# Performance work log

Measured on AMD Instinct MI355X. Metric: run time of the kernel, lower is better.

## Reference

```python
import jax, jax.numpy as jnp
import numpy as np
from itertools import combinations, product

NQ = 10
DIM = 2 ** NQ
DEPTH = 1
ENC_PAIRS = [(q, q + 1) for q in range(0, NQ - 1, 2)] + [(q, q + 1) for q in range(1, NQ - 1, 2)]  # brick layer: even then odd
PYR = [(i, i + 1) for layer in range(NQ - 1) for i in range(NQ - layer - 1)]  # pyramid RBS wire pairs (45)
OBS_PAIRS = list(combinations(range(NQ), 2))  # 45 pairwise 2-local observables

_P = {'I': np.eye(2, dtype=np.complex128),
      'X': np.array([[0, 1], [1, 0]], dtype=np.complex128),
      'Y': np.array([[0, -1j], [1j, 0]], dtype=np.complex128),
      'Z': np.array([[1, 0], [0, -1]], dtype=np.complex128)}
_WORDS = [''.join(w) for w in product('IXYZ', repeat=2)][1:]  # PennyLane pauli_basis order, identity excluded
P15 = jnp.asarray(np.stack([np.kron(_P[w[0]], _P[w[1]]) for w in _WORDS]).astype(np.complex64))
XXm = jnp.asarray(np.kron(_P['X'], _P['X']).astype(np.complex64))
YYm = jnp.asarray(np.kron(_P['Y'], _P['Y']).astype(np.complex64))
ZZm = jnp.asarray(np.kron(_P['Z'], _P['Z']).astype(np.complex64))
I4 = jnp.eye(4, dtype=jnp.complex64)
_TRIL_I, _TRIL_J = np.tril_indices(4, -1)  # order matches create_Hermitian's count+j indexing


def _u3(t, p, l):
    c = jnp.cos(t / 2).astype(jnp.complex64)
    s = jnp.sin(t / 2).astype(jnp.complex64)
    return jnp.stack([jnp.stack([c, -jnp.exp(1j * l) * s]),
                      jnp.stack([jnp.exp(1j * p) * s, jnp.exp(1j * (p + l)) * c])])


def _ising(phi, P):
    # exp(-i*phi/2 * P) for P in {XX, YY, ZZ} (P^2 = I)
    return jnp.cos(phi / 2) * I4 - 1j * jnp.sin(phi / 2) * P


def _apply1(psi, U, w):
    # psi: (B, 2, ..., 2); single-qubit gate U (2,2) on wire w
    psi = jnp.moveaxis(psi, 1 + w, -1)
    sh = psi.shape
    out = jnp.einsum('ij,brj->bri', U, psi.reshape(sh[0], -1, 2)).reshape(sh)
    return jnp.moveaxis(out, -1, 1 + w)


def _apply2(psi, U, a, b):
    # two-qubit gate on wires (a,b), a is most-significant (PennyLane wire order). U: (4,4) or batched (B,4,4)
    psi = jnp.moveaxis(psi, (1 + a, 1 + b), (-2, -1))
    sh = psi.shape
    flat = psi.reshape(sh[0], -1, 4)
    eq = 'bij,brj->bri' if U.ndim == 3 else 'ij,brj->bri'
    out = jnp.einsum(eq, U, flat).reshape(sh)
    return jnp.moveaxis(out, (-2, -1), (1 + a, 1 + b))


def _build_H(A, B, D):
    # create_Hermitian: lower triangle A+iB, diag[0:3] = D[1:4], diag[3]=0, then h + h^dagger
    n = A.shape[0]
    h = jnp.zeros((n, 4, 4), jnp.complex64)
    h = h.at[:, _TRIL_I, _TRIL_J].set(A.astype(jnp.complex64) + 1j * B.astype(jnp.complex64))
    d = np.arange(3)
    h = h.at[:, d, d].set(D[:, 1:4].astype(jnp.complex64))
    return h + jnp.conj(jnp.swapaxes(h, -1, -2))


def setup_inputs() -> dict:
    key = jax.random.key(0)
    ks = jax.random.split(key, 9)
    f32 = jnp.float32
    return {
        'x': jax.random.normal(ks[0], (256, 512), f32),
        'W1': jax.random.normal(ks[1], (512, 256), f32) * (512 ** -0.5),
        'b1': jnp.zeros((256,), f32),
        'W2': jax.random.normal(ks[2], (256, 135), f32) * (256 ** -0.5),
        'b2': jnp.zeros((135,), f32),
        'qvit_params': 0.01 * jax.random.normal(ks[3], (DEPTH, len(PYR), 12), f32),
        'A': 2.0 * jax.random.normal(ks[4], (len(OBS_PAIRS), 6), f32),
        'B': 2.0 * jax.random.normal(ks[5], (len(OBS_PAIRS), 6), f32),
        'D': 2.0 * jax.random.normal(ks[6], (len(OBS_PAIRS), 4), f32),
    }


def reference(x, W1, b1, W2, b2, qvit_params, A, B, D):
    Bsz = x.shape[0]
    # enc_proj: Linear -> SiLU -> Linear
    enc = jax.nn.silu(x @ W1 + b1) @ W2 + b2  # (B, 135)
    # Brick-layer SpecialUnitary encoding: U = exp(i * sum theta_m P_m) via eigh
    theta = enc.reshape(Bsz, len(ENC_PAIRS), 15).astype(jnp.complex64)
    Hg = jnp.einsum('bgm,mij->bgij', theta, P15)  # Hermitian generators (B, 9, 4, 4)
    ew, V = jnp.linalg.eigh(Hg)
    Ue = jnp.einsum('bgik,bgk,bgjk->bgij', V, jnp.exp(1j * ew.astype(jnp.complex64)), jnp.conj(V))
    # |0...0>
    psi = jnp.zeros((Bsz, DIM), jnp.complex64).at[:, 0].set(1.0).reshape((Bsz,) + (2,) * NQ)
    for g, (a, b) in enumerate(ENC_PAIRS):
        psi = _apply2(psi, Ue[:, g], a, b)
    # QViT pyramid ansatz
    for ly in range(DEPTH):
        for g, (a, b) in enumerate(PYR):
            p = qvit_params[ly, g]
            psi = _apply1(psi, _u3(p[0], p[1], p[2]), a)
            psi = _apply2(psi, _ising(p[3], XXm), a, b)
            psi = _apply2(psi, _ising(p[4], YYm), a, b)
            psi = _apply2(psi, _ising(p[5], ZZm), a, b)
            psi = _apply1(psi, _u3(p[6], p[7], p[8]), a)
            psi = _apply2(psi, _ising(p[9], XXm), a, b)
            psi = _apply2(psi, _ising(p[10], YYm), a, b)
            psi = _apply2(psi, _ising(p[11], ZZm), a, b)
    # Pairwise ANO Hermitian expectations
    Hobs = _build_H(A, B, D)  # (45, 4, 4)
    outs = []
    for w, (a, b) in enumerate(OBS_PAIRS):
        pm = jnp.moveaxis(psi, (1 + a, 1 + b), (1, 2)).reshape(Bsz, 4, -1)
        outs.append(jnp.real(jnp.einsum('bir,ij,bjr->b', jnp.conj(pm), Hobs[w], pm)))
    return jnp.stack(outs, axis=1).astype(jnp.float32)
```

## Files before the change

### kernel.cpp

```cpp
#include <hip/hip_runtime.h>
#include <math.h>

#define NOBS 45
typedef float2 c32;

__device__ __constant__ int PA_s[NOBS] = {
    1,1,1,1,1,1,1,1,1, 0,0,0,0,0,0,0,0, 7,7,7,7,7,7,7, 6,6,6,6,6,6,
    5,5,5,5,5, 3,3,3,3, 2,2,2, 4,4, 9};
__device__ __constant__ int PB_s[NOBS] = {
    0,7,6,5,3,2,4,9,8, 7,6,5,3,2,4,9,8, 6,5,3,2,4,9,8, 5,3,2,4,9,8,
    3,2,4,9,8, 2,4,9,8, 4,9,8, 9,8, 8};
constexpr int TIc[6] = {1, 2, 2, 3, 3, 3};
constexpr int TJc[6] = {0, 0, 1, 0, 1, 2};

__device__ __forceinline__ c32 cfma(c32 a, c32 b, c32 c) {
    c.x = fmaf(a.x, b.x, fmaf(-a.y, b.y, c.x));
    c.y = fmaf(a.x, b.y, fmaf(a.y, b.x, c.y));
    return c;
}
__device__ __forceinline__ c32 cmul(c32 a, c32 b) {
    return make_float2(a.x * b.x - a.y * b.y, a.x * b.y + a.y * b.x);
}

template <int CTRL>
__device__ __forceinline__ float dppf(float x) {
    return __uint_as_float((unsigned)__builtin_amdgcn_update_dpp(
        0, (int)__float_as_uint(x), CTRL, 0xF, 0xF, true));
}
__device__ __forceinline__ float swap32f(float a) {
    auto r = __builtin_amdgcn_permlane32_swap(__float_as_uint(a), __float_as_uint(a), false, false);
    return (__uint_as_float(r[0]) + __uint_as_float(r[1])) - a;
}
#if __has_builtin(__builtin_amdgcn_permlane16_swap)
__device__ __forceinline__ float swap16f(float a) {
    auto r = __builtin_amdgcn_permlane16_swap(__float_as_uint(a), __float_as_uint(a), false, false);
    return (__uint_as_float(r[0]) + __uint_as_float(r[1])) - a;
}
#else
__device__ __forceinline__ float swap16f(float a) { return __shfl_xor(a, 16, 64); }
#endif
__device__ __forceinline__ float swz4f(float a) {
    return __uint_as_float(__builtin_amdgcn_ds_swizzle(__float_as_uint(a), 0x101F));
}
template <int M>
__device__ __forceinline__ float exf(float x) {
    float r = x;
    if constexpr ((M & 3) == 1) r = dppf<0xB1>(r);
    else if constexpr ((M & 3) == 2) r = dppf<0x4E>(r);
    else if constexpr ((M & 3) == 3) r = dppf<0x1B>(r);
    if constexpr (M & 4)  r = swz4f(r);
    if constexpr (M & 8)  r = dppf<0x128>(r);
    if constexpr (M & 16) r = swap16f(r);
    if constexpr (M & 32) r = swap32f(r);
    return r;
}
template <int M>
__device__ __forceinline__ c32 exch(c32 a) { return make_float2(exf<M>(a.x), exf<M>(a.y)); }
__device__ __forceinline__ c32 swap32c(c32 a) { return make_float2(swap32f(a.x), swap32f(a.y)); }

__device__ __forceinline__ float wave_reduce63(float x) {
    x += dppf<0x111>(x);
    x += dppf<0x112>(x);
    x += dppf<0x114>(x);
    x += dppf<0x118>(x);
    x += dppf<0x142>(x);
    x += dppf<0x143>(x);
    return x;
}

__device__ __forceinline__ int insert2(int t, int pl, int ph) {
    int low  = t & ((1 << pl) - 1);
    int rest = t >> pl;
    int nm   = ph - 1 - pl;
    int mid  = rest & ((1 << nm) - 1);
    int high = rest >> nm;
    return low | (mid << (pl + 1)) | (high << (ph + 1));
}

template <int W>
__device__ __forceinline__ c32 pE(int r, int c) {
    if constexpr (W == 0) return make_float2((r == c) ? 1.f : 0.f, 0.f);
    else if constexpr (W == 1) return make_float2((r != c) ? 1.f : 0.f, 0.f);
    else if constexpr (W == 2) return make_float2(0.f, (r == c) ? 0.f : ((r == 0) ? -1.f : 1.f));
    else return make_float2((r == c) ? ((r == 0) ? 1.f : -1.f) : 0.f, 0.f);
}
template <int W0, int W1>
__device__ __forceinline__ void paccum(c32& H, float th, int i1, int i2, int j1, int j2) {
    c32 a = pE<W0>(i1, j1), b = pE<W1>(i2, j2);
    c32 p = cmul(a, b);
    H.x = fmaf(th, p.x, H.x);
    H.y = fmaf(th, p.y, H.y);
}

struct F16 { c32 u[16]; };
struct FLoc { c32 a[4]; c32 b[4]; };
struct F4 { c32 uS, uB, uA, uC; };

__device__ __forceinline__ F16 loadF16(const c32* __restrict__ U) {
    F16 f;
#pragma unroll
    for (int i = 0; i < 16; i++) f.u[i] = U[i];
    return f;
}
__device__ __forceinline__ FLoc loadLoc(const c32* __restrict__ U, int ln) {
    int bb = (ln >> 5) & 1;
    const c32* U0 = U + bb * 4;
    const c32* U1 = U + (2 | bb) * 4;
    int c00 = bb, c01 = 2 | bb, c10 = bb ^ 1, c11 = 2 | (bb ^ 1);
    FLoc f;
    f.a[0] = U0[c00]; f.a[1] = U0[c01]; f.a[2] = U0[c10]; f.a[3] = U0[c11];
    f.b[0] = U1[c00]; f.b[1] = U1[c01]; f.b[2] = U1[c10]; f.b[3] = U1[c11];
    return f;
}
template <int QA, int QB>
__device__ __forceinline__ F4 loadL2(const c32* __restrict__ U, int ln) {
    int bA = (ln >> QA) & 1, bB = (ln >> QB) & 1;
    int r = (bA << 1) | bB;
    const c32* Ur = U + r * 4;
    F4 f;
    f.uS = Ur[r]; f.uB = Ur[r ^ 1]; f.uA = Ur[r ^ 2]; f.uC = Ur[r ^ 3];
    return f;
}

__device__ __forceinline__ void applyLL(c32 v[4], const F16& f) {
    c32 n0 = cfma(f.u[0],  v[0], cfma(f.u[1],  v[1], cfma(f.u[2],  v[2], cmul(f.u[3],  v[3]))));
    c32 n1 = cfma(f.u[4],  v[0], cfma(f.u[5],  v[1], cfma(f.u[6],  v[2], cmul(f.u[7],  v[3]))));
    c32 n2 = cfma(f.u[8],  v[0], cfma(f.u[9],  v[1], cfma(f.u[10], v[2], cmul(f.u[11], v[3]))));
    c32 n3 = cfma(f.u[12], v[0], cfma(f.u[13], v[1], cfma(f.u[14], v[2], cmul(f.u[15], v[3]))));
    v[0] = n0; v[1] = n1; v[2] = n2; v[3] = n3;
}
__device__ __forceinline__ void applyLoc(c32 v[4], const FLoc& f) {
    c32 p0 = swap32c(v[0]), p1 = swap32c(v[1]), p2 = swap32c(v[2]), p3 = swap32c(v[3]);
    c32 n0 = cfma(f.a[0], v[0], cfma(f.a[1], v[1], cfma(f.a[2], p0, cmul(f.a[3], p1))));
    c32 n1 = cfma(f.b[0], v[0], cfma(f.b[1], v[1], cfma(f.b[2], p0, cmul(f.b[3], p1))));
    c32 n2 = cfma(f.a[0], v[2], cfma(f.a[1], v[3], cfma(f.a[2], p2, cmul(f.a[3], p3))));
    c32 n3 = cfma(f.b[0], v[2], cfma(f.b[1], v[3], cfma(f.b[2], p2, cmul(f.b[3], p3))));
    v[0] = n0; v[1] = n1; v[2] = n2; v[3] = n3;
}
template <int QA, int QB>
__device__ __forceinline__ void applyL2(c32 v[4], const F4& f) {
#pragma unroll
    for (int lc = 0; lc < 4; lc++) {
        c32 pB = exch<(1 << QB)>(v[lc]);
        c32 pA = exch<(1 << QA)>(v[lc]);
        c32 pC = exch<(1 << QA)>(pB);
        v[lc] = cfma(f.uS, v[lc], cfma(f.uB, pB, cfma(f.uA, pA, cmul(f.uC, pC))));
    }
}

__device__ __forceinline__ void dumpV(const c32 v[4], c32* __restrict__ psi, int t) {
#pragma unroll
    for (int lc = 0; lc < 4; lc++) psi[(t << 2) | lc] = v[lc];
}
__device__ __forceinline__ void loadV(c32 v[4], const c32* __restrict__ psi, int t) {
#pragma unroll
    for (int lc = 0; lc < 4; lc++) v[lc] = psi[(t << 2) | lc];
}
template <int PA, int PB>
__device__ __forceinline__ void ldsApply(const F16& f, c32* __restrict__ psi, int t) {
    constexpr int PL = (PA < PB) ? PA : PB, PH = (PA < PB) ? PB : PA;
    int base = insert2(t, PL, PH);
    constexpr int oa = 1 << PA, ob = 1 << PB;
    c32 g0 = psi[base], g1 = psi[base + ob], g2 = psi[base + oa], g3 = psi[base + oa + ob];
    c32 n0 = cfma(f.u[0],  g0, cfma(f.u[1],  g1, cfma(f.u[2],  g2, cmul(f.u[3],  g3))));
    c32 n1 = cfma(f.u[4],  g0, cfma(f.u[5],  g1, cfma(f.u[6],  g2, cmul(f.u[7],  g3))));
    c32 n2 = cfma(f.u[8],  g0, cfma(f.u[9],  g1, cfma(f.u[10], g2, cmul(f.u[11], g3))));
    c32 n3 = cfma(f.u[12], g0, cfma(f.u[13], g1, cfma(f.u[14], g2, cmul(f.u[15], g3))));
    psi[base] = n0; psi[base + ob] = n1; psi[base + oa] = n2; psi[base + oa + ob] = n3;
}

__global__ __launch_bounds__(256, 1) void mega_kernel(
    const float* __restrict__ x,  const float* __restrict__ W1, const float* __restrict__ b1,
    const float* __restrict__ W2, const float* __restrict__ b2, const float* __restrict__ qp,
    const float* __restrict__ Am, const float* __restrict__ Bm, const float* __restrict__ Dm,
    float* __restrict__ out) {
    __shared__ __align__(16) c32 psiS[1024];
    __shared__ c32 UeS[144];
    __shared__ c32 GpS[720];
    __shared__ float HbS[720];
    __shared__ float encS[136];
    __shared__ float redS[180];

    const int b = blockIdx.x, t = threadIdx.x, ln = t & 63;
    float* F = (float*)psiS;

    if (t < 128) ((float4*)F)[t] = ((const float4*)(x + (size_t)b * 512))[t];
    __syncthreads();
    {
        int q = t & 63, sl = t >> 6;
        float4 a4 = make_float4(0.f, 0.f, 0.f, 0.f);
#pragma unroll 16
        for (int kk = 0; kk < 128; kk++) {
            int k = sl * 128 + kk;
            float xk = F[k];
            const float4 w = *(const float4*)(W1 + (size_t)k * 256 + q * 4);
            a4.x = fmaf(xk, w.x, a4.x); a4.y = fmaf(xk, w.y, a4.y);
            a4.z = fmaf(xk, w.z, a4.z); a4.w = fmaf(xk, w.w, a4.w);
        }
        *(float4*)(F + 512 + sl * 256 + q * 4) = a4;
    }
    __syncthreads();
    {
        float hv = b1[t] + F[512 + t] + F[768 + t] + F[1024 + t] + F[1280 + t];
        hv = hv / (1.f + __expf(-hv));
        F[1536 + t] = hv;
    }
    __syncthreads();
    if (t < 135) {
        float a2 = b2[t], a3 = 0.f;
#pragma unroll 16
        for (int k = 0; k < 128; k++) {
            a2 = fmaf(F[1536 + k],       W2[(size_t)k * 135 + t],         a2);
            a3 = fmaf(F[1536 + 128 + k], W2[(size_t)(128 + k) * 135 + t], a3);
        }
        encS[t] = a2 + a3;
    }
    __syncthreads();

    c32* Mm = psiS;
    c32* Rb = psiS + 144;
    c32* TA = psiS + 288;
    if (t < 144) {
        int m = t >> 4, e = t & 15, i = e >> 2, j = e & 3;
        int i1 = i >> 1, i2 = i & 1, j1 = j >> 1, j2 = j & 1;
        const float* th = encS + m * 15;
        c32 H = make_float2(0.f, 0.f);
        paccum<0,1>(H, th[0],  i1,i2,j1,j2); paccum<0,2>(H, th[1],  i1,i2,j1,j2);
        paccum<0,3>(H, th[2],  i1,i2,j1,j2); paccum<1,0>(H, th[3],  i1,i2,j1,j2);
        paccum<1,1>(H, th[4],  i1,i2,j1,j2); paccum<1,2>(H, th[5],  i1,i2,j1,j2);
        paccum<1,3>(H, th[6],  i1,i2,j1,j2); paccum<2,0>(H, th[7],  i1,i2,j1,j2);
        paccum<2,1>(H, th[8],  i1,i2,j1,j2); paccum<2,2>(H, th[9],  i1,i2,j1,j2);
        paccum<2,3>(H, th[10], i1,i2,j1,j2); paccum<3,0>(H, th[11], i1,i2,j1,j2);
        paccum<3,1>(H, th[12], i1,i2,j1,j2); paccum<3,2>(H, th[13], i1,i2,j1,j2);
        paccum<3,3>(H, th[14], i1,i2,j1,j2);
        const float sc = 1.f / 64.f;
        Mm[t] = make_float2(-H.y * sc, H.x * sc);
        Rb[t] = make_float2((i == j) ? 1.f : 0.f, 0.f);
    } else if (t >= 234) {
        for (int w = t - 234; w < NOBS; w += 22) {
            float* Hf = HbS + w * 16;
            Hf[0] = 2.f * Dm[w * 4 + 1];
            Hf[1] = 2.f * Dm[w * 4 + 2];
            Hf[2] = 2.f * Dm[w * 4 + 3];
            Hf[3] = 0.f;
#pragma unroll
            for (int k = 0; k < 6; k++) {
                Hf[4 + 2 * k] = 2.f * Am[w * 6 + k];
                Hf[5 + 2 * k] = 2.f * Bm[w * 6 + k];
            }
        }
    }
    __syncthreads();
    c32 Mrow[4];
    if (t < 144) {
        int m = t >> 4, i = (t & 15) >> 2;
#pragma unroll
        for (int k = 0; k < 4; k++) Mrow[k] = Mm[m * 16 + i * 4 + k];
    }
#pragma unroll 1
    for (int step = 0; step < 13; step++) {
        if (t < 144) {
            int m = t >> 4, e = t & 15, i = e >> 2, j = e & 3;
            const c32* cur = (step & 1) ? UeS : Rb;
            c32 acc = make_float2(0.f, 0.f);
            c32 outv;
            if (step < 7) {
#pragma unroll
                for (int k = 0; k < 4; k++) acc = cfma(Mrow[k], cur[m * 16 + k * 4 + j], acc);
                float inv = 1.f / (float)(7 - step);
                outv = make_float2(fmaf(acc.x, inv, (i == j) ? 1.f : 0.f), acc.y * inv);
            } else {
#pragma unroll
                for (int k = 0; k < 4; k++)
                    acc = cfma(cur[m * 16 + i * 4 + k], cur[m * 16 + k * 4 + j], acc);
                outv = acc;
            }
            ((step & 1) ? Rb : UeS)[t] = outv;
        } else if (t >= 144 && t < 234 && step < 8) {
            int pt = t - 144, g = pt >> 1, ih = (pt & 1) << 1;
            const float* p = qp + g * 12;
            const c32* src = ((step & 1) ? TA : GpS) + g * 16;
            c32* dst = ((step & 1) ? GpS : TA) + g * 16;
#pragma unroll
            for (int r2 = 0; r2 < 2; r2++) {
                int i = ih + r2, i1 = i >> 1, i2 = i & 1;
                c32 row[4];
                if (step == 0) {
                    float s, c; __sincosf(p[0] * 0.5f, &s, &c);
                    c32 u0, u1;
                    if (i1 == 0) { u0 = make_float2(c, 0.f);
                                   u1 = make_float2(-__cosf(p[2]) * s, -__sinf(p[2]) * s); }
                    else { u0 = make_float2(__cosf(p[1]) * s, __sinf(p[1]) * s);
                           u1 = make_float2(__cosf(p[1] + p[2]) * c, __sinf(p[1] + p[2]) * c); }
#pragma unroll
                    for (int jj = 0; jj < 4; jj++) row[jj] = make_float2(0.f, 0.f);
                    row[i2] = u0; row[2 | i2] = u1;
                } else {
                    c32 coef0, coef1; int c0, c1;
                    if (step == 1 || step == 5) {
                        float s, c; __sincosf(p[step == 1 ? 3 : 9] * 0.5f, &s, &c);
                        c0 = i; coef0 = make_float2(c, 0.f);
                        c1 = i ^ 3; coef1 = make_float2(0.f, -s);
                    } else if (step == 2 || step == 6) {
                        float s, c; __sincosf(p[step == 2 ? 4 : 10] * 0.5f, &s, &c);
                        float yy = (i == 0 || i == 3) ? 1.f : -1.f;
                        c0 = i; coef0 = make_float2(c, 0.f);
                        c1 = i ^ 3; coef1 = make_float2(0.f, s * yy);
                    } else if (step == 3 || step == 7) {
                        float s, c; __sincosf(p[step == 3 ? 5 : 11] * 0.5f, &s, &c);
                        float zz = (i == 0 || i == 3) ? 1.f : -1.f;
                        c0 = i; coef0 = make_float2(c, -s * zz);
                        c1 = i; coef1 = make_float2(0.f, 0.f);
                    } else {
                        float s, c; __sincosf(p[6] * 0.5f, &s, &c);
                        if (i1 == 0) { coef0 = make_float2(c, 0.f);
                                       coef1 = make_float2(-__cosf(p[8]) * s, -__sinf(p[8]) * s); }
                        else { coef0 = make_float2(__cosf(p[7]) * s, __sinf(p[7]) * s);
                               coef1 = make_float2(__cosf(p[7] + p[8]) * c, __sinf(p[7] + p[8]) * c); }
                        c0 = i2; c1 = 2 | i2;
                    }
#pragma unroll
                    for (int jj = 0; jj < 4; jj++)
                        row[jj] = cfma(coef0, src[c0 * 4 + jj], cmul(coef1, src[c1 * 4 + jj]));
                }
#pragma unroll
                for (int jj = 0; jj < 4; jj++) dst[i * 4 + jj] = row[jj];
            }
        }
        __syncthreads();
    }

    c32 v[4];
#pragma unroll
    for (int lc = 0; lc < 4; lc++) v[lc] = make_float2(0.f, 0.f);
    if (t == 0) v[0] = make_float2(1.f, 0.f);

    applyLL(v, loadF16(UeS + 0));
    applyL2<5, 4>(v, loadL2<5, 4>(UeS + 16, ln));
    applyL2<3, 1>(v, loadL2<3, 1>(UeS + 32, ln));
    applyL2<0, 2>(v, loadL2<0, 2>(UeS + 48, ln));
    dumpV(v, psiS, t); __syncthreads();
    ldsApply<9, 8>(loadF16(UeS + 64), psiS, t); __syncthreads();
    loadV(v, psiS, t);
    applyLoc(v, loadLoc(UeS + 80, ln));
    applyL2<4, 3>(v, loadL2<4, 3>(UeS + 96, ln));
    applyL2<1, 0>(v, loadL2<1, 0>(UeS + 112, ln));
    dumpV(v, psiS, t); __syncthreads();
    ldsApply<4, 9>(loadF16(UeS + 128), psiS, t); __syncthreads();
    loadV(v, psiS, t);

    {
        int g = 0;
#pragma unroll 1
        for (int layer = 0; layer < 9; layer++) {
            const int amax = 8 - layer;
            applyLL(v, loadF16(GpS + (g++) * 16));
            if (amax >= 1) applyLoc(v, loadLoc(GpS + (g++) * 16, ln));
            if (amax >= 2) applyL2<5, 4>(v, loadL2<5, 4>(GpS + (g++) * 16, ln));
            if (amax >= 3) applyL2<4, 3>(v, loadL2<4, 3>(GpS + (g++) * 16, ln));
            if (amax >= 4) applyL2<3, 1>(v, loadL2<3, 1>(GpS + (g++) * 16, ln));
            if (amax >= 5) applyL2<1, 0>(v, loadL2<1, 0>(GpS + (g++) * 16, ln));
            if (amax >= 6) applyL2<0, 2>(v, loadL2<0, 2>(GpS + (g++) * 16, ln));
            if (amax >= 7) {
                dumpV(v, psiS, t); __syncthreads();
                ldsApply<4, 9>(loadF16(GpS + (g++) * 16), psiS, t); __syncthreads();
                if (amax >= 8) {
                    ldsApply<9, 8>(loadF16(GpS + (g++) * 16), psiS, t); __syncthreads();
                }
                loadV(v, psiS, t);
            }
        }
    }

    dumpV(v, psiS, t);
    __syncthreads();
#pragma unroll 1
    for (int w0 = 0; w0 < NOBS; w0 += 5) {
        float pr[5];
#pragma unroll
        for (int u = 0; u < 5; u++) {
            const int w = w0 + u;
            const int pa = PA_s[w], pb = PB_s[w];
            const int pl = (pa < pb) ? pa : pb, phh = (pa < pb) ? pb : pa;
            const int oa = 1 << pa, ob = 1 << pb;
            int i0 = insert2(t, pl, phh);
            c32 vg[4];
            vg[0] = psiS[i0];      vg[1] = psiS[i0 + ob];
            vg[2] = psiS[i0 + oa]; vg[3] = psiS[i0 + oa + ob];
            const float* Hf = HbS + w * 16;
            float r = Hf[0] * fmaf(vg[0].x, vg[0].x, vg[0].y * vg[0].y)
                    + Hf[1] * fmaf(vg[1].x, vg[1].x, vg[1].y * vg[1].y)
                    + Hf[2] * fmaf(vg[2].x, vg[2].x, vg[2].y * vg[2].y);
#pragma unroll
            for (int k = 0; k < 6; k++) {
                c32 vi = vg[TIc[k]], vj = vg[TJc[k]];
                float cx = fmaf(vi.x, vj.x, vi.y * vj.y);
                float cy = fmaf(vi.x, vj.y, -vi.y * vj.x);
                r = fmaf(Hf[4 + 2 * k], cx, r);
                r = fmaf(-Hf[5 + 2 * k], cy, r);
            }
            pr[u] = wave_reduce63(r);
        }
        if (ln == 63) {
#pragma unroll
            for (int u = 0; u < 5; u++) redS[(w0 + u) * 4 + (t >> 6)] = pr[u];
        }
    }
    __syncthreads();
    if (t < NOBS)
        out[(size_t)b * NOBS + t] = redS[t * 4] + redS[t * 4 + 1] + redS[t * 4 + 2] + redS[t * 4 + 3];
}

extern "C" void kernel_launch(void* const* d_in, const int* in_sizes, int n_in,
                              void* d_out, int out_size, void* d_ws, size_t ws_size,
                              hipStream_t stream) {
    (void)in_sizes; (void)n_in; (void)out_size; (void)d_ws; (void)ws_size;
    const float* x  = (const float*)d_in[0];
    const float* W1 = (const float*)d_in[1];
    const float* b1 = (const float*)d_in[2];
    const float* W2 = (const float*)d_in[3];
    const float* b2 = (const float*)d_in[4];
    const float* qp = (const float*)d_in[5];
    const float* Am = (const float*)d_in[6];
    const float* Bm = (const float*)d_in[7];
    const float* Dm = (const float*)d_in[8];
    float* out = (float*)d_out;

    hipLaunchKernelGGL(mega_kernel, dim3(256), dim3(256), 0, stream,
                       x, W1, b1, W2, b2, qp, Am, Bm, Dm, out);
}
```

Measured before the change: 112.2 us.

## Replace LDS-synchronized prologue matrix builds with in-register swizzle math and unroll loops

The encoder-unitary series and squaring now run entirely in registers, using ds_swizzle row/column exchanges across the 16 lanes that hold each 4x4 matrix. This removes the 13 shared-memory steps, each ending in a block barrier. The per-gate fused unitaries are now built by one thread per gate in registers instead of by 8 synchronized steps. The gate and observable loops are fully unrolled, with the observable wire indices turned into compile-time constants. FMA chains are also reordered, and the W2 dot product is split into four accumulators. Full unrolling can raise code size and register pressure, and the single-thread gate builds serialize work that used to be spread across threads.

```diff
diff --git a/kernel.cpp b/kernel.cpp
--- a/kernel.cpp
+++ b/kernel.cpp
@@ -4,12 +4,13 @@
 #define NOBS 45
 typedef float2 c32;
 
-__device__ __constant__ int PA_s[NOBS] = {
-    1,1,1,1,1,1,1,1,1, 0,0,0,0,0,0,0,0, 7,7,7,7,7,7,7, 6,6,6,6,6,6,
-    5,5,5,5,5, 3,3,3,3, 2,2,2, 4,4, 9};
-__device__ __constant__ int PB_s[NOBS] = {
-    0,7,6,5,3,2,4,9,8, 7,6,5,3,2,4,9,8, 6,5,3,2,4,9,8, 5,3,2,4,9,8,
-    3,2,4,9,8, 2,4,9,8, 4,9,8, 9,8, 8};
+constexpr int W2Sc[10] = {1, 0, 7, 6, 5, 3, 2, 4, 9, 8};
+constexpr int OAc[NOBS] = {
+    0,0,0,0,0,0,0,0,0, 1,1,1,1,1,1,1,1, 2,2,2,2,2,2,2, 3,3,3,3,3,3,
+    4,4,4,4,4, 5,5,5,5, 6,6,6, 7,7, 8};
+constexpr int OBc[NOBS] = {
+    1,2,3,4,5,6,7,8,9, 2,3,4,5,6,7,8,9, 3,4,5,6,7,8,9, 4,5,6,7,8,9,
+    5,6,7,8,9, 6,7,8,9, 7,8,9, 8,9, 9};
 constexpr int TIc[6] = {1, 2, 2, 3, 3, 3};
 constexpr int TJc[6] = {0, 0, 1, 0, 1, 2};
 
@@ -39,8 +40,9 @@
 #else
 __device__ __forceinline__ float swap16f(float a) { return __shfl_xor(a, 16, 64); }
 #endif
-__device__ __forceinline__ float swz4f(float a) {
-    return __uint_as_float(__builtin_amdgcn_ds_swizzle(__float_as_uint(a), 0x101F));
+template <int OFF>
+__device__ __forceinline__ float swzf(float a) {
+    return __uint_as_float(__builtin_amdgcn_ds_swizzle(__float_as_uint(a), OFF));
 }
 template <int M>
 __device__ __forceinline__ float exf(float x) {
@@ -48,7 +50,7 @@
     if constexpr ((M & 3) == 1) r = dppf<0xB1>(r);
     else if constexpr ((M & 3) == 2) r = dppf<0x4E>(r);
     else if constexpr ((M & 3) == 3) r = dppf<0x1B>(r);
-    if constexpr (M & 4)  r = swz4f(r);
+    if constexpr (M & 4)  r = swzf<0x101F>(r);
     if constexpr (M & 8)  r = dppf<0x128>(r);
     if constexpr (M & 16) r = swap16f(r);
     if constexpr (M & 32) r = swap32f(r);
@@ -57,6 +59,17 @@
 template <int M>
 __device__ __forceinline__ c32 exch(c32 a) { return make_float2(exf<M>(a.x), exf<M>(a.y)); }
 __device__ __forceinline__ c32 swap32c(c32 a) { return make_float2(swap32f(a.x), swap32f(a.y)); }
+
+template <int K>
+__device__ __forceinline__ c32 swzrow(c32 a) {
+    constexpr int off = (K << 5) | 0x1C;
+    return make_float2(swzf<off>(a.x), swzf<off>(a.y));
+}
+template <int K>
+__device__ __forceinline__ c32 swzcol(c32 a) {
+    constexpr int off = ((K << 2) << 5) | 0x13;
+    return make_float2(swzf<off>(a.x), swzf<off>(a.y));
+}
 
 __device__ __forceinline__ float wave_reduce63(float x) {
     x += dppf<0x111>(x);
@@ -90,6 +103,65 @@
     c32 p = cmul(a, b);
     H.x = fmaf(th, p.x, H.x);
     H.y = fmaf(th, p.y, H.y);
+}
+
+__device__ __forceinline__ void buildU3kron(c32* d, float th, float ph, float la) {
+    float s, c; __sincosf(th * 0.5f, &s, &c);
+    c32 u00 = make_float2(c, 0.f);
+    c32 u01 = make_float2(-__cosf(la) * s, -__sinf(la) * s);
+    c32 u10 = make_float2(__cosf(ph) * s, __sinf(ph) * s);
+    c32 u11 = make_float2(__cosf(ph + la) * c, __sinf(ph + la) * c);
+#pragma unroll
+    for (int i = 0; i < 16; i++) d[i] = make_float2(0.f, 0.f);
+    d[0] = u00; d[2] = u01; d[5] = u00; d[7] = u01;
+    d[8] = u10; d[10] = u11; d[13] = u10; d[15] = u11;
+}
+__device__ __forceinline__ void stepXX(c32* d, const c32* sM, float phi) {
+    float s, c; __sincosf(phi * 0.5f, &s, &c);
+    c32 k1 = make_float2(0.f, -s);
+#pragma unroll
+    for (int i = 0; i < 4; i++)
+#pragma unroll
+        for (int j = 0; j < 4; j++)
+            d[i * 4 + j] = cfma(k1, sM[(i ^ 3) * 4 + j],
+                                make_float2(c * sM[i * 4 + j].x, c * sM[i * 4 + j].y));
+}
+__device__ __forceinline__ void stepYY(c32* d, const c32* sM, float phi) {
+    float s, c; __sincosf(phi * 0.5f, &s, &c);
+#pragma unroll
+    for (int i = 0; i < 4; i++) {
+        float yy = (i == 0 || i == 3) ? 1.f : -1.f;
+        c32 k1 = make_float2(0.f, s * yy);
+#pragma unroll
+        for (int j = 0; j < 4; j++)
+            d[i * 4 + j] = cfma(k1, sM[(i ^ 3) * 4 + j],
+                                make_float2(c * sM[i * 4 + j].x, c * sM[i * 4 + j].y));
+    }
+}
+__device__ __forceinline__ void stepZZ(c32* d, const c32* sM, float phi) {
+    float s, c; __sincosf(phi * 0.5f, &s, &c);
+#pragma unroll
+    for (int i = 0; i < 4; i++) {
+        float zz = (i == 0 || i == 3) ? 1.f : -1.f;
+        c32 k = make_float2(c, -s * zz);
+#pragma unroll
+        for (int j = 0; j < 4; j++) d[i * 4 + j] = cmul(k, sM[i * 4 + j]);
+    }
+}
+__device__ __forceinline__ void stepU3(c32* d, const c32* sM, float th, float ph, float la) {
+    float s, c; __sincosf(th * 0.5f, &s, &c);
+    c32 u00 = make_float2(c, 0.f);
+    c32 u01 = make_float2(-__cosf(la) * s, -__sinf(la) * s);
+    c32 u10 = make_float2(__cosf(ph) * s, __sinf(ph) * s);
+    c32 u11 = make_float2(__cosf(ph + la) * c, __sinf(ph + la) * c);
+#pragma unroll
+    for (int i = 0; i < 4; i++) {
+        int i1 = i >> 1, i2 = i & 1;
+        c32 c0 = i1 ? u10 : u00, c1 = i1 ? u11 : u01;
+#pragma unroll
+        for (int j = 0; j < 4; j++)
+            d[i * 4 + j] = cfma(c0, sM[i2 * 4 + j], cmul(c1, sM[(2 | i2) * 4 + j]));
+    }
 }
 
 struct F16 { c32 u[16]; };
@@ -123,29 +195,32 @@
 }
 
 __device__ __forceinline__ void applyLL(c32 v[4], const F16& f) {
-    c32 n0 = cfma(f.u[0],  v[0], cfma(f.u[1],  v[1], cfma(f.u[2],  v[2], cmul(f.u[3],  v[3]))));
-    c32 n1 = cfma(f.u[4],  v[0], cfma(f.u[5],  v[1], cfma(f.u[6],  v[2], cmul(f.u[7],  v[3]))));
-    c32 n2 = cfma(f.u[8],  v[0], cfma(f.u[9],  v[1], cfma(f.u[10], v[2], cmul(f.u[11], v[3]))));
-    c32 n3 = cfma(f.u[12], v[0], cfma(f.u[13], v[1], cfma(f.u[14], v[2], cmul(f.u[15], v[3]))));
+    c32 n0 = cfma(f.u[3],  v[3], cfma(f.u[2],  v[2], cfma(f.u[1],  v[1], cmul(f.u[0],  v[0]))));
+    c32 n1 = cfma(f.u[7],  v[3], cfma(f.u[6],  v[2], cfma(f.u[5],  v[1], cmul(f.u[4],  v[0]))));
+    c32 n2 = cfma(f.u[11], v[3], cfma(f.u[10], v[2], cfma(f.u[9],  v[1], cmul(f.u[8],  v[0]))));
+    c32 n3 = cfma(f.u[15], v[3], cfma(f.u[14], v[2], cfma(f.u[13], v[1], cmul(f.u[12], v[0]))));
     v[0] = n0; v[1] = n1; v[2] = n2; v[3] = n3;
 }
 __device__ __forceinline__ void applyLoc(c32 v[4], const FLoc& f) {
     c32 p0 = swap32c(v[0]), p1 = swap32c(v[1]), p2 = swap32c(v[2]), p3 = swap32c(v[3]);
-    c32 n0 = cfma(f.a[0], v[0], cfma(f.a[1], v[1], cfma(f.a[2], p0, cmul(f.a[3], p1))));
-    c32 n1 = cfma(f.b[0], v[0], cfma(f.b[1], v[1], cfma(f.b[2], p0, cmul(f.b[3], p1))));
-    c32 n2 = cfma(f.a[0], v[2], cfma(f.a[1], v[3], cfma(f.a[2], p2, cmul(f.a[3], p3))));
-    c32 n3 = cfma(f.b[0], v[2], cfma(f.b[1], v[3], cfma(f.b[2], p2, cmul(f.b[3], p3))));
+    c32 n0 = cfma(f.a[3], p1, cfma(f.a[2], p0, cfma(f.a[1], v[1], cmul(f.a[0], v[0]))));
+    c32 n1 = cfma(f.b[3], p1, cfma(f.b[2], p0, cfma(f.b[1], v[1], cmul(f.b[0], v[0]))));
+    c32 n2 = cfma(f.a[3], p3, cfma(f.a[2], p2, cfma(f.a[1], v[3], cmul(f.a[0], v[2]))));
+    c32 n3 = cfma(f.b[3], p3, cfma(f.b[2], p2, cfma(f.b[1], v[3], cmul(f.b[0], v[2]))));
     v[0] = n0; v[1] = n1; v[2] = n2; v[3] = n3;
 }
 template <int QA, int QB>
 __device__ __forceinline__ void applyL2(c32 v[4], const F4& f) {
-#pragma unroll
-    for (int lc = 0; lc < 4; lc++) {
-        c32 pB = exch<(1 << QB)>(v[lc]);
-        c32 pA = exch<(1 << QA)>(v[lc]);
-        c32 pC = exch<(1 << QA)>(pB);
-        v[lc] = cfma(f.uS, v[lc], cfma(f.uB, pB, cfma(f.uA, pA, cmul(f.uC, pC))));
-    }
+    c32 pB[4], pA[4], pC[4];
+#pragma unroll
+    for (int lc = 0; lc < 4; lc++) pB[lc] = exch<(1 << QB)>(v[lc]);
+#pragma unroll
+    for (int lc = 0; lc < 4; lc++) pA[lc] = exch<(1 << QA)>(v[lc]);
+#pragma unroll
+    for (int lc = 0; lc < 4; lc++) pC[lc] = exch<(1 << QA)>(pB[lc]);
+#pragma unroll
+    for (int lc = 0; lc < 4; lc++)
+        v[lc] = cfma(f.uC, pC[lc], cfma(f.uA, pA[lc], cfma(f.uB, pB[lc], cmul(f.uS, v[lc]))));
 }
 
 __device__ __forceinline__ void dumpV(const c32 v[4], c32* __restrict__ psi, int t) {
@@ -162,10 +237,10 @@
     int base = insert2(t, PL, PH);
     constexpr int oa = 1 << PA, ob = 1 << PB;
     c32 g0 = psi[base], g1 = psi[base + ob], g2 = psi[base + oa], g3 = psi[base + oa + ob];
-    c32 n0 = cfma(f.u[0],  g0, cfma(f.u[1],  g1, cfma(f.u[2],  g2, cmul(f.u[3],  g3))));
-    c32 n1 = cfma(f.u[4],  g0, cfma(f.u[5],  g1, cfma(f.u[6],  g2, cmul(f.u[7],  g3))));
-    c32 n2 = cfma(f.u[8],  g0, cfma(f.u[9],  g1, cfma(f.u[10], g2, cmul(f.u[11], g3))));
-    c32 n3 = cfma(f.u[12], g0, cfma(f.u[13], g1, cfma(f.u[14], g2, cmul(f.u[15], g3))));
+    c32 n0 = cfma(f.u[3],  g3, cfma(f.u[2],  g2, cfma(f.u[1],  g1, cmul(f.u[0],  g0))));
+    c32 n1 = cfma(f.u[7],  g3, cfma(f.u[6],  g2, cfma(f.u[5],  g1, cmul(f.u[4],  g0))));
+    c32 n2 = cfma(f.u[11], g3, cfma(f.u[10], g2, cfma(f.u[9],  g1, cmul(f.u[8],  g0))));
+    c32 n3 = cfma(f.u[15], g3, cfma(f.u[14], g2, cfma(f.u[13], g1, cmul(f.u[12], g0))));
     psi[base] = n0; psi[base + ob] = n1; psi[base + oa] = n2; psi[base + oa + ob] = n3;
 }
 
@@ -207,23 +282,23 @@
     }
     __syncthreads();
     if (t < 135) {
-        float a2 = b2[t], a3 = 0.f;
+        float a0 = b2[t], a1 = 0.f, a2 = 0.f, a3 = 0.f;
 #pragma unroll 16
-        for (int k = 0; k < 128; k++) {
-            a2 = fmaf(F[1536 + k],       W2[(size_t)k * 135 + t],         a2);
-            a3 = fmaf(F[1536 + 128 + k], W2[(size_t)(128 + k) * 135 + t], a3);
-        }
-        encS[t] = a2 + a3;
-    }
-    __syncthreads();
-
-    c32* Mm = psiS;
-    c32* Rb = psiS + 144;
-    c32* TA = psiS + 288;
+        for (int k = 0; k < 64; k++) {
+            a0 = fmaf(F[1536 + k],       W2[(size_t)k * 135 + t],         a0);
+            a1 = fmaf(F[1536 + 64 + k],  W2[(size_t)(64 + k) * 135 + t],  a1);
+            a2 = fmaf(F[1536 + 128 + k], W2[(size_t)(128 + k) * 135 + t], a2);
+            a3 = fmaf(F[1536 + 192 + k], W2[(size_t)(192 + k) * 135 + t], a3);
+        }
+        encS[t] = (a0 + a1) + (a2 + a3);
+    }
+    __syncthreads();
+
     if (t < 144) {
-        int m = t >> 4, e = t & 15, i = e >> 2, j = e & 3;
-        int i1 = i >> 1, i2 = i & 1, j1 = j >> 1, j2 = j & 1;
-        const float* th = encS + m * 15;
+        const int e = t & 15, i = e >> 2, j = e & 3;
+        const int i1 = i >> 1, i2 = i & 1, j1 = j >> 1, j2 = j & 1;
+        const float idq = (i == j) ? 1.f : 0.f;
+        const float* th = encS + (t >> 4) * 15;
         c32 H = make_float2(0.f, 0.f);
         paccum<0,1>(H, th[0],  i1,i2,j1,j2); paccum<0,2>(H, th[1],  i1,i2,j1,j2);
         paccum<0,3>(H, th[2],  i1,i2,j1,j2); paccum<1,0>(H, th[3],  i1,i2,j1,j2);
@@ -234,101 +309,54 @@
         paccum<3,1>(H, th[12], i1,i2,j1,j2); paccum<3,2>(H, th[13], i1,i2,j1,j2);
         paccum<3,3>(H, th[14], i1,i2,j1,j2);
         const float sc = 1.f / 64.f;
-        Mm[t] = make_float2(-H.y * sc, H.x * sc);
-        Rb[t] = make_float2((i == j) ? 1.f : 0.f, 0.f);
-    } else if (t >= 234) {
-        for (int w = t - 234; w < NOBS; w += 22) {
-            float* Hf = HbS + w * 16;
-            Hf[0] = 2.f * Dm[w * 4 + 1];
-            Hf[1] = 2.f * Dm[w * 4 + 2];
-            Hf[2] = 2.f * Dm[w * 4 + 3];
-            Hf[3] = 0.f;
-#pragma unroll
-            for (int k = 0; k < 6; k++) {
-                Hf[4 + 2 * k] = 2.f * Am[w * 6 + k];
-                Hf[5 + 2 * k] = 2.f * Bm[w * 6 + k];
-            }
-        }
-    }
-    __syncthreads();
-    c32 Mrow[4];
-    if (t < 144) {
-        int m = t >> 4, i = (t & 15) >> 2;
-#pragma unroll
-        for (int k = 0; k < 4; k++) Mrow[k] = Mm[m * 16 + i * 4 + k];
-    }
+        const c32 M = make_float2(-H.y * sc, H.x * sc);
+        c32 R = make_float2(idq, 0.f);
 #pragma unroll 1
-    for (int step = 0; step < 13; step++) {
-        if (t < 144) {
-            int m = t >> 4, e = t & 15, i = e >> 2, j = e & 3;
-            const c32* cur = (step & 1) ? UeS : Rb;
-            c32 acc = make_float2(0.f, 0.f);
-            c32 outv;
-            if (step < 7) {
-#pragma unroll
-                for (int k = 0; k < 4; k++) acc = cfma(Mrow[k], cur[m * 16 + k * 4 + j], acc);
-                float inv = 1.f / (float)(7 - step);
-                outv = make_float2(fmaf(acc.x, inv, (i == j) ? 1.f : 0.f), acc.y * inv);
-            } else {
-#pragma unroll
-                for (int k = 0; k < 4; k++)
-                    acc = cfma(cur[m * 16 + i * 4 + k], cur[m * 16 + k * 4 + j], acc);
-                outv = acc;
-            }
-            ((step & 1) ? Rb : UeS)[t] = outv;
-        } else if (t >= 144 && t < 234 && step < 8) {
-            int pt = t - 144, g = pt >> 1, ih = (pt & 1) << 1;
-            const float* p = qp + g * 12;
-            const c32* src = ((step & 1) ? TA : GpS) + g * 16;
-            c32* dst = ((step & 1) ? GpS : TA) + g * 16;
-#pragma unroll
-            for (int r2 = 0; r2 < 2; r2++) {
-                int i = ih + r2, i1 = i >> 1, i2 = i & 1;
-                c32 row[4];
-                if (step == 0) {
-                    float s, c; __sincosf(p[0] * 0.5f, &s, &c);
-                    c32 u0, u1;
-                    if (i1 == 0) { u0 = make_float2(c, 0.f);
-                                   u1 = make_float2(-__cosf(p[2]) * s, -__sinf(p[2]) * s); }
-                    else { u0 = make_float2(__cosf(p[1]) * s, __sinf(p[1]) * s);
-                           u1 = make_float2(__cosf(p[1] + p[2]) * c, __sinf(p[1] + p[2]) * c); }
-#pragma unroll
-                    for (int jj = 0; jj < 4; jj++) row[jj] = make_float2(0.f, 0.f);
-                    row[i2] = u0; row[2 | i2] = u1;
-                } else {
-                    c32 coef0, coef1; int c0, c1;
-                    if (step == 1 || step == 5) {
-                        float s, c; __sincosf(p[step == 1 ? 3 : 9] * 0.5f, &s, &c);
-                        c0 = i; coef0 = make_float2(c, 0.f);
-                        c1 = i ^ 3; coef1 = make_float2(0.f, -s);
-                    } else if (step == 2 || step == 6) {
-                        float s, c; __sincosf(p[step == 2 ? 4 : 10] * 0.5f, &s, &c);
-                        float yy = (i == 0 || i == 3) ? 1.f : -1.f;
-                        c0 = i; coef0 = make_float2(c, 0.f);
-                        c1 = i ^ 3; coef1 = make_float2(0.f, s * yy);
-                    } else if (step == 3 || step == 7) {
-                        float s, c; __sincosf(p[step == 3 ? 5 : 11] * 0.5f, &s, &c);
-                        float zz = (i == 0 || i == 3) ? 1.f : -1.f;
-                        c0 = i; coef0 = make_float2(c, -s * zz);
-                        c1 = i; coef1 = make_float2(0.f, 0.f);
-                    } else {
-                        float s, c; __sincosf(p[6] * 0.5f, &s, &c);
-                        if (i1 == 0) { coef0 = make_float2(c, 0.f);
-                                       coef1 = make_float2(-__cosf(p[8]) * s, -__sinf(p[8]) * s); }
-                        else { coef0 = make_float2(__cosf(p[7]) * s, __sinf(p[7]) * s);
-                               coef1 = make_float2(__cosf(p[7] + p[8]) * c, __sinf(p[7] + p[8]) * c); }
-                        c0 = i2; c1 = 2 | i2;
-                    }
-#pragma unroll
-                    for (int jj = 0; jj < 4; jj++)
-                        row[jj] = cfma(coef0, src[c0 * 4 + jj], cmul(coef1, src[c1 * 4 + jj]));
-                }
-#pragma unroll
-                for (int jj = 0; jj < 4; jj++) dst[i * 4 + jj] = row[jj];
-            }
-        }
-        __syncthreads();
-    }
+        for (int step = 0; step < 7; step++) {
+            c32 acc = cmul(swzrow<0>(M), swzcol<0>(R));
+            acc = cfma(swzrow<1>(M), swzcol<1>(R), acc);
+            acc = cfma(swzrow<2>(M), swzcol<2>(R), acc);
+            acc = cfma(swzrow<3>(M), swzcol<3>(R), acc);
+            float inv = 1.f / (float)(7 - step);
+            R = make_float2(fmaf(acc.x, inv, idq), acc.y * inv);
+        }
+#pragma unroll 1
+        for (int sq = 0; sq < 6; sq++) {
+            c32 acc = cmul(swzrow<0>(R), swzcol<0>(R));
+            acc = cfma(swzrow<1>(R), swzcol<1>(R), acc);
+            acc = cfma(swzrow<2>(R), swzcol<2>(R), acc);
+            acc = cfma(swzrow<3>(R), swzcol<3>(R), acc);
+            R = acc;
+        }
+        UeS[t] = R;
+    } else if (t < 189) {
+        const int w = t - 144;
+        float* Hf = HbS + w * 16;
+        Hf[0] = 2.f * Dm[w * 4 + 1];
+        Hf[1] = 2.f * Dm[w * 4 + 2];
+        Hf[2] = 2.f * Dm[w * 4 + 3];
+        Hf[3] = 0.f;
+#pragma unroll
+        for (int k = 0; k < 6; k++) {
+            Hf[4 + 2 * k] = 2.f * Am[w * 6 + k];
+            Hf[5 + 2 * k] = 2.f * Bm[w * 6 + k];
+        }
+    } else if (t >= 192 && t < 237) {
+        const int g = t - 192;
+        const float* p = qp + g * 12;
+        c32 A[16], Bt[16];
+        buildU3kron(A, p[0], p[1], p[2]);
+        stepXX(Bt, A, p[3]);
+        stepYY(A, Bt, p[4]);
+        stepZZ(Bt, A, p[5]);
+        stepU3(A, Bt, p[6], p[7], p[8]);
+        stepXX(Bt, A, p[9]);
+        stepYY(A, Bt, p[10]);
+        stepZZ(Bt, A, p[11]);
+#pragma unroll
+        for (int k = 0; k < 16; k++) GpS[g * 16 + k] = Bt[k];
+    }
+    __syncthreads();
 
     c32 v[4];
 #pragma unroll
@@ -351,7 +379,7 @@
 
     {
         int g = 0;
-#pragma unroll 1
+#pragma unroll
         for (int layer = 0; layer < 9; layer++) {
             const int amax = 8 - layer;
             applyLL(v, loadF16(GpS + (g++) * 16));
@@ -374,13 +402,13 @@
 
     dumpV(v, psiS, t);
     __syncthreads();
-#pragma unroll 1
+#pragma unroll
     for (int w0 = 0; w0 < NOBS; w0 += 5) {
         float pr[5];
 #pragma unroll
         for (int u = 0; u < 5; u++) {
             const int w = w0 + u;
-            const int pa = PA_s[w], pb = PB_s[w];
+            const int pa = W2Sc[OAc[w]], pb = W2Sc[OBc[w]];
             const int pl = (pa < pb) ? pa : pb, phh = (pa < pb) ? pb : pa;
             const int oa = 1 << pa, ob = 1 << pb;
             int i0 = insert2(t, pl, phh);
```

New measurement: 106.6 us. 5.1% less time.
